# Performance work log

Hardware: AMD Instinct MI355X
Metric: run time of the kernel (lower is better)

## Reference

```python
import jax, jax.numpy as jnp
import numpy as np

N_NODES = 100000
N_EDGES = 20000
NNZ = 600000
N_GRAPHS = 64
IN_C, HID_C, OUT_C = 128, 128, 16


def setup_inputs() -> dict:
    key = jax.random.key(0)
    ks = jax.random.split(key, 10)
    x = jax.random.normal(ks[0], (N_NODES, IN_C), dtype=jnp.float32)
    node_idx = jax.random.randint(ks[1], (NNZ,), 0, N_NODES)
    edge_idx = jax.random.randint(ks[2], (NNZ,), 0, N_EDGES)
    batch = jnp.sort(jax.random.randint(ks[3], (N_NODES,), 0, N_GRAPHS))
    s1 = 1.0 / np.sqrt(IN_C)
    s2 = 1.0 / np.sqrt(HID_C)
    W1 = jax.random.uniform(ks[4], (IN_C, HID_C), jnp.float32, -s1, s1)
    b1 = jnp.zeros((HID_C,), jnp.float32)
    W2 = jax.random.uniform(ks[5], (HID_C, HID_C), jnp.float32, -s2, s2)
    b2 = jnp.zeros((HID_C,), jnp.float32)
    Wfc = jax.random.uniform(ks[6], (HID_C, OUT_C), jnp.float32, -s2, s2)
    bfc = jax.random.uniform(ks[7], (OUT_C,), jnp.float32, -s2, s2)
    return {"x": x, "node_idx": node_idx, "edge_idx": edge_idx, "batch": batch,
            "W1": W1, "b1": b1, "W2": W2, "b2": b2, "Wfc": Wfc, "bfc": bfc}


def hypergraph_conv(x, node_idx, edge_idx, W, b):
    # x' = D^{-1} H B^{-1} H^T (x W) + b   (unit hyperedge weights)
    x = x @ W  # lin has bias=False in PyG HypergraphConv
    ones = jnp.ones((node_idx.shape[0],), x.dtype)
    De = jax.ops.segment_sum(ones, edge_idx, num_segments=N_EDGES)   # hyperedge degree
    Dn = jax.ops.segment_sum(ones, node_idx, num_segments=N_NODES)  # node degree
    Binv = jnp.where(De > 0, 1.0 / De, 0.0)[:, None]
    Dinv = jnp.where(Dn > 0, 1.0 / Dn, 0.0)[:, None]
    # node -> hyperedge aggregation
    e = jax.ops.segment_sum(x[node_idx], edge_idx, num_segments=N_EDGES) * Binv
    # hyperedge -> node aggregation
    out = jax.ops.segment_sum(e[edge_idx], node_idx, num_segments=N_NODES) * Dinv
    return out + b


def reference(x, node_idx, edge_idx, batch, W1, b1, W2, b2, Wfc, bfc):
    h = jax.nn.relu(hypergraph_conv(x, node_idx, edge_idx, W1, b1))
    h = jax.nn.relu(hypergraph_conv(h, node_idx, edge_idx, W2, b2))
    # global mean pool over graphs
    cnt = jax.ops.segment_sum(jnp.ones((N_NODES,), h.dtype), batch, num_segments=N_GRAPHS)
    pooled = jax.ops.segment_sum(h, batch, num_segments=N_GRAPHS) / jnp.maximum(cnt, 1.0)[:, None]
    logits = pooled @ Wfc + bfc
    return jax.nn.log_softmax(logits, axis=1)
```

## Files before the change

### kernel.cpp

```cpp
#include <hip/hip_runtime.h>

#define N_NODES  100000
#define N_EDGES  20000
#define NNZ_     600000
#define N_GRAPHS 64
#define C_       128

typedef unsigned short ushort_t;
typedef unsigned int   uint_t;
typedef unsigned char  uchar_t;
typedef __attribute__((ext_vector_type(4))) float f32x4;
typedef __attribute__((ext_vector_type(2))) float f32x2;

__device__ __forceinline__ ushort_t f2bf(float f) {
    uint_t u = __float_as_uint(f);
    u += 0x7fffu + ((u >> 16) & 1u);
    return (ushort_t)(u >> 16);
}


#define SORT_ITEMS 2048
#define BKT_CAP    16384
#define NBKT_E     40
#define NBKT_N     49
#define SB_        ((NNZ_ + SORT_ITEMS - 1) / SORT_ITEMS)
#define CONV_XBLKS 6250
#define CONV_WBLKS 64

__global__ __launch_bounds__(256) void scatter_conv(const int* __restrict__ node_idx,
                                                    const int* __restrict__ edge_idx,
                                                    int* __restrict__ bcur,
                                                    int2* __restrict__ stage_e,
                                                    int2* __restrict__ stage_n,
                                                    const float* __restrict__ X, uint_t* __restrict__ X8,
                                                    const float* __restrict__ W1, const float* __restrict__ W2,
                                                    uchar_t* __restrict__ WT1, uchar_t* __restrict__ WT2) {
    __shared__ int cnt[NBKT_N];
    __shared__ int base[NBKT_N];
    __shared__ int gbase[NBKT_N];
    __shared__ int2 buf[SORT_ITEMS];
    int t = threadIdx.x;
    int bxx = blockIdx.x;

    if (bxx >= SB_) {
        int bx = bxx - SB_;
        if (bx < CONV_XBLKS) {
            size_t c = (size_t)bx * 256 + t;
            size_t bb = c * 8;
            if (bb >= (size_t)N_NODES * C_) return;
            float4 f0 = *(const float4*)(X + bb);
            float4 f1 = *(const float4*)(X + bb + 4);
            uint_t w0 = 0, w1 = 0;
            w0 = __builtin_amdgcn_cvt_pk_fp8_f32(f0.x, f0.y, w0, 0);
            w0 = __builtin_amdgcn_cvt_pk_fp8_f32(f0.z, f0.w, w0, 1);
            w1 = __builtin_amdgcn_cvt_pk_fp8_f32(f1.x, f1.y, w1, 0);
            w1 = __builtin_amdgcn_cvt_pk_fp8_f32(f1.z, f1.w, w1, 1);
            uint2 o; o.x = w0; o.y = w1;
            *(uint2*)(X8 + c * 2) = o;
        } else {
            bx -= CONV_XBLKS;
            const float* W = (bx < 32) ? W1 : W2;
            uchar_t* WT    = (bx < 32) ? WT1 : WT2;
            int idx = (bx & 31) * 256 + t;
            int n = idx >> 6, k2 = (idx & 63) * 2;
            float a = W[k2 * 128 + n];
            float b = W[(k2 + 1) * 128 + n];
            uint_t p = __builtin_amdgcn_cvt_pk_fp8_f32(a, b, 0, 0);
            *(ushort_t*)(WT + n * 128 + k2) = (ushort_t)(p & 0xffff);
        }
        return;
    }

    int start = bxx * SORT_ITEMS;
    int nitems = min(SORT_ITEMS, NNZ_ - start);

    int ek[8], nk[8];
    #pragma unroll
    for (int j = 0; j < 8; j++) {
        int i = t + j * 256;
        if (i < nitems) { ek[j] = edge_idx[start + i]; nk[j] = node_idx[start + i]; }
    }

    #pragma unroll
    for (int side = 0; side < 2; side++) {
        const int SHIFT = side ? 11 : 9;
        const int NBKT  = side ? NBKT_N : NBKT_E;
        int2* stage = side ? stage_n : stage_e;
        int*  bc    = bcur + side * 64;

        if (side) __syncthreads();
        for (int i = t; i < NBKT; i += 256) cnt[i] = 0;
        __syncthreads();

        int rank[8], bkt[8];
        #pragma unroll
        for (int j = 0; j < 8; j++) {
            int i = t + j * 256;
            if (i < nitems) {
                int key = side ? nk[j] : ek[j];
                bkt[j]  = key >> SHIFT;
                rank[j] = atomicAdd(&cnt[bkt[j]], 1);
            }
        }
        __syncthreads();
        if (t < 64) {
            int v = (t < NBKT) ? cnt[t] : 0;
            int s = v;
            #pragma unroll
            for (int o = 1; o < 64; o <<= 1) { int u = __shfl_up(s, o); if (t >= o) s += u; }
            if (t < NBKT) base[t] = s - v;
        }
        __syncthreads();
        if (t < NBKT) {
            int c = cnt[t];
            gbase[t] = t * BKT_CAP + ((c > 0) ? atomicAdd(&bc[t], c) : 0);
        }
        #pragma unroll
        for (int j = 0; j < 8; j++) {
            int i = t + j * 256;
            if (i < nitems) {
                int key = side ? nk[j] : ek[j];
                int val = side ? ek[j] : nk[j];
                buf[base[bkt[j]] + rank[j]] = make_int2(key, val);
            }
        }
        __syncthreads();
        for (int i = t; i < nitems; i += 256) {
            int2 p = buf[i];
            int b = p.x >> SHIFT;
            stage[gbase[b] + (i - base[b])] = p;
        }
    }
}

__global__ __launch_bounds__(1024) void bucket_build(const int2* __restrict__ stage_e,
                                                     const int2* __restrict__ stage_n,
                                                     const int* __restrict__ bcur,
                                                     int* __restrict__ ecnt, int* __restrict__ ncnt,
                                                     int* __restrict__ eoffs, int* __restrict__ noffs,
                                                     float* __restrict__ binv, float* __restrict__ dinv,
                                                     int* __restrict__ csr_en, int* __restrict__ csr_ne) {
    __shared__ int hist[2048];
    __shared__ int offs[2048];
    __shared__ int wsum[16];
    __shared__ int sbase;
    int t = threadIdx.x;
    int bx = blockIdx.x;
    const int2* sb; int* cnt; int* koffs; float* inv; int* csr;
    const int* bc; int b, width, nkeys, nb, k0;
    if (bx < NBKT_E) {
        b = bx; bc = bcur;
        sb = stage_e + (size_t)b * BKT_CAP; cnt = ecnt; koffs = eoffs; inv = binv; csr = csr_en;
        k0 = b << 9; width = 512; nkeys = N_EDGES; nb = NBKT_E;
    } else {
        b = bx - NBKT_E; bc = bcur + 64;
        sb = stage_n + (size_t)b * BKT_CAP; cnt = ncnt; koffs = noffs; inv = dinv; csr = csr_ne;
        k0 = b << 11; width = 2048; nkeys = N_NODES; nb = NBKT_N;
    }
    int n = bc[b];
    if (t < 64) {
        int v = (t < nb) ? bc[t] : 0;
        int s = v;
        #pragma unroll
        for (int o = 1; o < 64; o <<= 1) { int u = __shfl_up(s, o); if (t >= o) s += u; }
        if (t == b) sbase = s - v;
    }
    for (int i = t; i < width; i += 1024) hist[i] = 0;
    __syncthreads();
    for (int i = t; i < n; i += 1024) atomicAdd(&hist[sb[i].x - k0], 1);
    __syncthreads();
    int e0 = 0, e1 = 0;
    if (2 * t < width) { e0 = hist[2 * t]; e1 = hist[2 * t + 1]; }
    int s = e0 + e1;
    int lane = t & 63, wv = t >> 6;
    int sc = s;
    #pragma unroll
    for (int o = 1; o < 64; o <<= 1) { int u = __shfl_up(sc, o); if (lane >= o) sc += u; }
    if (lane == 63) wsum[wv] = sc;
    __syncthreads();
    if (t < 16) {
        int v = wsum[t];
        int s2 = v;
        #pragma unroll
        for (int o = 1; o < 16; o <<= 1) { int u = __shfl_up(s2, o); if (t >= o) s2 += u; }
        wsum[t] = s2 - v;
    }
    __syncthreads();
    if (2 * t < width) {
        int excl = (sc - s) + wsum[wv];
        offs[2 * t]     = excl;
        offs[2 * t + 1] = excl + e0;
    }
    __syncthreads();
    int base_g = sbase;
    for (int i = t; i < width; i += 1024) {
        int k = k0 + i;
        if (k < nkeys) {
            int c = hist[i];
            cnt[k]   = c;
            koffs[k] = base_g + offs[i];
            inv[k]   = (c > 0) ? 1.0f / (float)c : 0.0f;
        }
    }
    __syncthreads();
    for (int i = t; i < n; i += 1024) {
        int2 p = sb[i];
        int pos = atomicAdd(&offs[p.x - k0], 1);
        csr[base_g + pos] = p.y;
    }
}


__global__ __launch_bounds__(256) void gemm_mfma8(const uchar_t* __restrict__ A8,
                                                  const uchar_t* __restrict__ WT8,
                                                  uchar_t* __restrict__ C8, int M) {
    __shared__ __align__(16) uchar_t Wl[128 * 128];
    __shared__ __align__(16) uchar_t Al[64 * 128];
    int t = threadIdx.x;
    int r0 = blockIdx.x * 64;

    const uint4* WTg = (const uint4*)WT8;
    #pragma unroll
    for (int i = 0; i < 4; i++) {
        int c = i * 256 + t;
        int row = c >> 3, col16 = (c & 7) * 16;
        *(uint4*)&Wl[row * 128 + (col16 ^ ((row & 7) << 4))] = WTg[c];
    }
    #pragma unroll
    for (int i = 0; i < 2; i++) {
        int c = i * 256 + t;
        int row = c >> 3, col16 = (c & 7) * 16;
        int gr = r0 + row; if (gr >= M) gr = M - 1;
        uint4 v = *(const uint4*)(A8 + (size_t)gr * 128 + col16);
        *(uint4*)&Al[row * 128 + (col16 ^ ((row & 7) << 4))] = v;
    }
    __syncthreads();

    int lane = t & 63, wid = t >> 6;
    int arow = wid * 16 + (lane & 15);
    int kq = lane >> 4;
    f32x4 acc[8] = {};

    #pragma unroll
    for (int ks = 0; ks < 4; ks++) {
        int colb = ks * 32 + kq * 8;
        long a = *(const long*)&Al[arow * 128 + (colb ^ ((arow & 7) << 4))];
        #pragma unroll
        for (int nt = 0; nt < 8; nt++) {
            int wr = nt * 16 + (lane & 15);
            long b = *(const long*)&Wl[wr * 128 + (colb ^ ((wr & 7) << 4))];
            acc[nt] = __builtin_amdgcn_mfma_f32_16x16x32_fp8_fp8(a, b, acc[nt], 0, 0, 0);
        }
    }

    __syncthreads();
    uchar_t* Cl = Al;
    #pragma unroll
    for (int nt = 0; nt < 8; nt++) {
        int col = nt * 16 + (lane & 15);
        #pragma unroll
        for (int j = 0; j < 4; j++) {
            int rl = wid * 16 + kq * 4 + j;
            uint_t p = __builtin_amdgcn_cvt_pk_fp8_f32(acc[nt][j], acc[nt][j], 0, 0);
            Cl[rl * 128 + col] = (uchar_t)(p & 0xff);
        }
    }
    __syncthreads();
    int rows_here = min(64, M - r0);
    uint4* dst = (uint4*)(C8 + (size_t)r0 * 128);
    const uint4* src = (const uint4*)Cl;
    for (int c = t; c < rows_here * 8; c += 256) dst[c] = src[c];
}


__device__ __forceinline__ void acc16(uint4 v, float* a) {
    f32x2 p0 = __builtin_amdgcn_cvt_pk_f32_fp8(v.x, 0);
    f32x2 p1 = __builtin_amdgcn_cvt_pk_f32_fp8(v.x, 1);
    f32x2 p2 = __builtin_amdgcn_cvt_pk_f32_fp8(v.y, 0);
    f32x2 p3 = __builtin_amdgcn_cvt_pk_f32_fp8(v.y, 1);
    f32x2 p4 = __builtin_amdgcn_cvt_pk_f32_fp8(v.z, 0);
    f32x2 p5 = __builtin_amdgcn_cvt_pk_f32_fp8(v.z, 1);
    f32x2 p6 = __builtin_amdgcn_cvt_pk_f32_fp8(v.w, 0);
    f32x2 p7 = __builtin_amdgcn_cvt_pk_f32_fp8(v.w, 1);
    a[0] += p0.x;  a[1] += p0.y;  a[2] += p1.x;  a[3] += p1.y;
    a[4] += p2.x;  a[5] += p2.y;  a[6] += p3.x;  a[7] += p3.y;
    a[8] += p4.x;  a[9] += p4.y;  a[10] += p5.x; a[11] += p5.y;
    a[12] += p6.x; a[13] += p6.y; a[14] += p7.x; a[15] += p7.y;
}

__device__ __forceinline__ uint4 pack16(const float* r) {
    uint_t w0 = __builtin_amdgcn_cvt_pk_fp8_f32(r[0],  r[1],  0, 0);
    w0 = __builtin_amdgcn_cvt_pk_fp8_f32(r[2],  r[3],  w0, 1);
    uint_t w1 = __builtin_amdgcn_cvt_pk_fp8_f32(r[4],  r[5],  0, 0);
    w1 = __builtin_amdgcn_cvt_pk_fp8_f32(r[6],  r[7],  w1, 1);
    uint_t w2 = __builtin_amdgcn_cvt_pk_fp8_f32(r[8],  r[9],  0, 0);
    w2 = __builtin_amdgcn_cvt_pk_fp8_f32(r[10], r[11], w2, 1);
    uint_t w3 = __builtin_amdgcn_cvt_pk_fp8_f32(r[12], r[13], 0, 0);
    w3 = __builtin_amdgcn_cvt_pk_fp8_f32(r[14], r[15], w3, 1);
    uint4 o; o.x = w0; o.y = w1; o.z = w2; o.w = w3;
    return o;
}

__global__ __launch_bounds__(256) void gather_edges8(const uint4* __restrict__ X,
                                                     const int* __restrict__ csr,
                                                     const int* __restrict__ off, const int* __restrict__ cnt,
                                                     const float* __restrict__ binv,
                                                     uint4* __restrict__ E8) {
    int g = (blockIdx.x * blockDim.x + threadIdx.x) >> 3;
    int l = threadIdx.x & 7;
    if (g >= N_EDGES) return;
    int s = off[g], n = cnt[g];
    float a[16] = {};
    int i = 0;
    for (; i + 8 <= n; i += 8) {
        int r0 = csr[s + i],     r1 = csr[s + i + 1], r2 = csr[s + i + 2], r3 = csr[s + i + 3];
        int r4 = csr[s + i + 4], r5 = csr[s + i + 5], r6 = csr[s + i + 6], r7 = csr[s + i + 7];
        uint4 v0 = X[(size_t)r0 * 8 + l];
        uint4 v1 = X[(size_t)r1 * 8 + l];
        uint4 v2 = X[(size_t)r2 * 8 + l];
        uint4 v3 = X[(size_t)r3 * 8 + l];
        uint4 v4 = X[(size_t)r4 * 8 + l];
        uint4 v5 = X[(size_t)r5 * 8 + l];
        uint4 v6 = X[(size_t)r6 * 8 + l];
        uint4 v7 = X[(size_t)r7 * 8 + l];
        acc16(v0, a); acc16(v1, a); acc16(v2, a); acc16(v3, a);
        acc16(v4, a); acc16(v5, a); acc16(v6, a); acc16(v7, a);
    }
    for (; i + 4 <= n; i += 4) {
        int r0 = csr[s + i], r1 = csr[s + i + 1], r2 = csr[s + i + 2], r3 = csr[s + i + 3];
        uint4 v0 = X[(size_t)r0 * 8 + l];
        uint4 v1 = X[(size_t)r1 * 8 + l];
        uint4 v2 = X[(size_t)r2 * 8 + l];
        uint4 v3 = X[(size_t)r3 * 8 + l];
        acc16(v0, a); acc16(v1, a); acc16(v2, a); acc16(v3, a);
    }
    for (; i < n; i++) {
        uint4 v = X[(size_t)csr[s + i] * 8 + l];
        acc16(v, a);
    }
    float sc = binv[g];
    float r[16];
    #pragma unroll
    for (int j = 0; j < 16; j++) r[j] = a[j] * sc;
    E8[(size_t)g * 8 + l] = pack16(r);
}

__global__ __launch_bounds__(256) void gather_nodes8(const uint4* __restrict__ F,
                                                     const int* __restrict__ csr,
                                                     const int* __restrict__ off, const int* __restrict__ cnt,
                                                     const float* __restrict__ dinv,
                                                     const float* __restrict__ bias,
                                                     uint4* __restrict__ Y) {
    int g = (blockIdx.x * blockDim.x + threadIdx.x) >> 3;
    int l = threadIdx.x & 7;
    if (g >= N_NODES) return;
    int s = off[g], n = cnt[g];
    float a[16] = {};
    int i = 0;
    for (; i + 4 <= n; i += 4) {
        int r0 = csr[s + i], r1 = csr[s + i + 1], r2 = csr[s + i + 2], r3 = csr[s + i + 3];
        uint4 v0 = F[(size_t)r0 * 8 + l];
        uint4 v1 = F[(size_t)r1 * 8 + l];
        uint4 v2 = F[(size_t)r2 * 8 + l];
        uint4 v3 = F[(size_t)r3 * 8 + l];
        acc16(v0, a); acc16(v1, a); acc16(v2, a); acc16(v3, a);
    }
    for (; i < n; i++) {
        uint4 v = F[(size_t)csr[s + i] * 8 + l];
        acc16(v, a);
    }
    float sc = dinv[g];
    const float4* bb = (const float4*)bias + l * 4;
    float4 b0 = bb[0], b1 = bb[1], b2 = bb[2], b3 = bb[3];
    float r[16];
    r[0]  = fmaxf(a[0]  * sc + b0.x, 0.f);
    r[1]  = fmaxf(a[1]  * sc + b0.y, 0.f);
    r[2]  = fmaxf(a[2]  * sc + b0.z, 0.f);
    r[3]  = fmaxf(a[3]  * sc + b0.w, 0.f);
    r[4]  = fmaxf(a[4]  * sc + b1.x, 0.f);
    r[5]  = fmaxf(a[5]  * sc + b1.y, 0.f);
    r[6]  = fmaxf(a[6]  * sc + b1.z, 0.f);
    r[7]  = fmaxf(a[7]  * sc + b1.w, 0.f);
    r[8]  = fmaxf(a[8]  * sc + b2.x, 0.f);
    r[9]  = fmaxf(a[9]  * sc + b2.y, 0.f);
    r[10] = fmaxf(a[10] * sc + b2.z, 0.f);
    r[11] = fmaxf(a[11] * sc + b2.w, 0.f);
    r[12] = fmaxf(a[12] * sc + b3.x, 0.f);
    r[13] = fmaxf(a[13] * sc + b3.y, 0.f);
    r[14] = fmaxf(a[14] * sc + b3.z, 0.f);
    r[15] = fmaxf(a[15] * sc + b3.w, 0.f);
    Y[(size_t)g * 8 + l] = pack16(r);
}


#define POOL_BLOCKS 1024

__global__ __launch_bounds__(256) void pool_kernel8(const ushort_t* __restrict__ H,
                                                    const int* __restrict__ batch,
                                                    float* __restrict__ P) {
    int wgid = blockIdx.x * 4 + (threadIdx.x >> 6);
    int lane = threadIdx.x & 63;
    const int NW = POOL_BLOCKS * 4;
    const int per = (N_NODES + NW - 1) / NW;
    int r0 = wgid * per;
    int r1 = min(r0 + per, N_NODES);
    if (r0 >= r1) return;
    float ax = 0.f, ay = 0.f;
    int g = batch[r0];
    int hiw = lane & 1;
    for (int r = r0; r < r1; r++) {
        int gr = batch[r];
        if (gr != g) {
            atomicAdd(&P[g * C_ + lane * 2],     ax);
            atomicAdd(&P[g * C_ + lane * 2 + 1], ay);
            ax = 0.f; ay = 0.f; g = gr;
        }
        uint_t v = ((const uint_t*)H)[(size_t)r * 32 + (lane >> 1)];
        f32x2 p = hiw ? __builtin_amdgcn_cvt_pk_f32_fp8(v, 1)
                      : __builtin_amdgcn_cvt_pk_f32_fp8(v, 0);
        ax += p.x; ay += p.y;
    }
    atomicAdd(&P[g * C_ + lane * 2],     ax);
    atomicAdd(&P[g * C_ + lane * 2 + 1], ay);
}

__device__ __forceinline__ int lower_bound_dev(const int* __restrict__ a, int n, int key) {
    int lo = 0, hi = n;
    while (lo < hi) { int mid = (lo + hi) >> 1; if (a[mid] < key) lo = mid + 1; else hi = mid; }
    return lo;
}

__global__ __launch_bounds__(1024) void final_kernel(const float* __restrict__ P, const int* __restrict__ batch,
                                                     const float* __restrict__ Wfc, const float* __restrict__ bfc,
                                                     float* __restrict__ out) {
    int t = threadIdx.x;
    int r = t >> 4, c = t & 15;
    int lo = lower_bound_dev(batch, N_NODES, r);
    int hi = lower_bound_dev(batch, N_NODES, r + 1);
    float cnt = (float)((hi - lo) > 0 ? (hi - lo) : 1);
    float acc = 0.f;
    #pragma unroll 8
    for (int k = 0; k < C_; k++) acc += P[r * C_ + k] * Wfc[k * 16 + c];
    float logit = acc / cnt + bfc[c];
    __shared__ float l[N_GRAPHS][16];
    l[r][c] = logit;
    __syncthreads();
    float m = -1e30f;
    #pragma unroll
    for (int k = 0; k < 16; k++) m = fmaxf(m, l[r][k]);
    float sum = 0.f;
    #pragma unroll
    for (int k = 0; k < 16; k++) sum += expf(l[r][k] - m);
    out[t] = logit - m - logf(sum);
}


extern "C" void kernel_launch(void* const* d_in, const int* in_sizes, int n_in,
                              void* d_out, int out_size, void* d_ws, size_t ws_size,
                              hipStream_t stream) {
    const float* x        = (const float*)d_in[0];
    const int*   node_idx = (const int*)  d_in[1];
    const int*   edge_idx = (const int*)  d_in[2];
    const int*   batch    = (const int*)  d_in[3];
    const float* W1       = (const float*)d_in[4];
    const float* b1       = (const float*)d_in[5];
    const float* W2       = (const float*)d_in[6];
    const float* b2       = (const float*)d_in[7];
    const float* Wfc      = (const float*)d_in[8];
    const float* bfc      = (const float*)d_in[9];
    float* out = (float*)d_out;

    char* ws = (char*)d_ws;
    size_t off = 0;
    auto alloc = [&](size_t bytes) -> char* {
        off = (off + 255) & ~(size_t)255;
        char* p = ws + off;
        off += bytes;
        return p;
    };

    uint_t* x8     = (uint_t*)  alloc((size_t)N_NODES * C_);
    uint_t* h8     = (uint_t*)  alloc((size_t)N_NODES * C_);
    uchar_t* Eb8   = (uchar_t*) alloc((size_t)N_EDGES * C_);
    uchar_t* Fb8   = (uchar_t*) alloc((size_t)N_EDGES * C_);
    uchar_t* wt1   = (uchar_t*) alloc((size_t)C_ * C_);
    uchar_t* wt2   = (uchar_t*) alloc((size_t)C_ * C_);
    int2*  stage_e = (int2*) alloc((size_t)NBKT_E * BKT_CAP * 8);
    int2*  stage_n = (int2*) alloc((size_t)NBKT_N * BKT_CAP * 8);
    int*   bcur   = (int*)  alloc((size_t)128 * 4);
    float* pooled = (float*)alloc((size_t)N_GRAPHS * C_ * 4);
    char*  zend   = ws + off;
    int*   ecnt   = (int*)  alloc((size_t)N_EDGES * 4);
    int*   ncnt   = (int*)  alloc((size_t)N_NODES * 4);
    int*   eoffs  = (int*)  alloc((size_t)N_EDGES * 4);
    int*   noffs  = (int*)  alloc((size_t)N_NODES * 4);
    int*   csr_en = (int*)  alloc((size_t)NNZ_ * 4);
    int*   csr_ne = (int*)  alloc((size_t)NNZ_ * 4);
    float* binv   = (float*)alloc((size_t)N_EDGES * 4);
    float* dinv   = (float*)alloc((size_t)N_NODES * 4);

    (void)hipMemsetAsync((void*)bcur, 0, (size_t)(zend - (char*)bcur), stream);

    scatter_conv<<<SB_ + CONV_XBLKS + CONV_WBLKS, 256, 0, stream>>>(
        node_idx, edge_idx, bcur, stage_e, stage_n, x, x8, W1, W2, wt1, wt2);
    bucket_build<<<NBKT_E + NBKT_N, 1024, 0, stream>>>(
        stage_e, stage_n, bcur, ecnt, ncnt, eoffs, noffs, binv, dinv, csr_en, csr_ne);

    const int GEB = (N_EDGES + 63) / 64;
    gather_edges8<<<N_EDGES * 8 / 256, 256, 0, stream>>>((const uint4*)x8, csr_en, eoffs, ecnt, binv,
                                                         (uint4*)Eb8);
    gemm_mfma8<<<GEB, 256, 0, stream>>>(Eb8, wt1, Fb8, N_EDGES);
    gather_nodes8<<<N_NODES * 8 / 256, 256, 0, stream>>>((const uint4*)Fb8, csr_ne, noffs, ncnt, dinv, b1,
                                                         (uint4*)h8);
    gather_edges8<<<N_EDGES * 8 / 256, 256, 0, stream>>>((const uint4*)h8, csr_en, eoffs, ecnt, binv,
                                                         (uint4*)Eb8);
    gemm_mfma8<<<GEB, 256, 0, stream>>>(Eb8, wt2, Fb8, N_EDGES);
    gather_nodes8<<<N_NODES * 8 / 256, 256, 0, stream>>>((const uint4*)Fb8, csr_ne, noffs, ncnt, dinv, b2,
                                                         (uint4*)x8);
    pool_kernel8<<<POOL_BLOCKS, 256, 0, stream>>>((const ushort_t*)x8, batch, pooled);
    final_kernel<<<1, 1024, 0, stream>>>(pooled, batch, Wfc, bfc, out);
}
```

Measured before the change: 157.7 us.

## Fuse final node gather with mean-pool accumulation via shared-memory partial sums

Replaces the last gather_nodes8 plus pool_kernel8 pair with one kernel. Each block gathers 32 nodes, applies scale, bias and ReLU, and accumulates the results into two per-graph shared buffers before a few global atomics. This removes the write and re-read of the final node features and one launch. The cost is many LDS atomics per node, and correctness relies on each 32-node block spanning at most two graphs, which holds only because batch is sorted and graphs are large.

New measurement: 202.9 us. 28.7% more time.

```diff
diff --git a/kernel.cpp b/kernel.cpp
--- a/kernel.cpp
+++ b/kernel.cpp
@@ -392,37 +392,76 @@
     Y[(size_t)g * 8 + l] = pack16(r);
 }
 
-
-#define POOL_BLOCKS 1024
-
-__global__ __launch_bounds__(256) void pool_kernel8(const ushort_t* __restrict__ H,
-                                                    const int* __restrict__ batch,
-                                                    float* __restrict__ P) {
-    int wgid = blockIdx.x * 4 + (threadIdx.x >> 6);
-    int lane = threadIdx.x & 63;
-    const int NW = POOL_BLOCKS * 4;
-    const int per = (N_NODES + NW - 1) / NW;
-    int r0 = wgid * per;
-    int r1 = min(r0 + per, N_NODES);
-    if (r0 >= r1) return;
-    float ax = 0.f, ay = 0.f;
-    int g = batch[r0];
-    int hiw = lane & 1;
-    for (int r = r0; r < r1; r++) {
-        int gr = batch[r];
-        if (gr != g) {
-            atomicAdd(&P[g * C_ + lane * 2],     ax);
-            atomicAdd(&P[g * C_ + lane * 2 + 1], ay);
-            ax = 0.f; ay = 0.f; g = gr;
-        }
-        uint_t v = ((const uint_t*)H)[(size_t)r * 32 + (lane >> 1)];
-        f32x2 p = hiw ? __builtin_amdgcn_cvt_pk_f32_fp8(v, 1)
-                      : __builtin_amdgcn_cvt_pk_f32_fp8(v, 0);
-        ax += p.x; ay += p.y;
-    }
-    atomicAdd(&P[g * C_ + lane * 2],     ax);
-    atomicAdd(&P[g * C_ + lane * 2 + 1], ay);
-}
+__global__ __launch_bounds__(256) void gather_nodes_pool(const uint4* __restrict__ F,
+                                                         const int* __restrict__ csr,
+                                                         const int* __restrict__ off,
+                                                         const int* __restrict__ cnt,
+                                                         const float* __restrict__ dinv,
+                                                         const float* __restrict__ bias,
+                                                         const int* __restrict__ batch,
+                                                         float* __restrict__ P) {
+    __shared__ float pbuf[2][C_];
+    int t = threadIdx.x;
+    int g0 = blockIdx.x * 32;
+    int g = g0 + (t >> 3);
+    int l = t & 7;
+    pbuf[t >> 7][t & 127] = 0.f;
+    __syncthreads();
+
+    int gfirst = batch[g0];
+    int glast  = batch[min(g0 + 31, N_NODES - 1)];
+
+    if (g < N_NODES) {
+        int s = off[g], n = cnt[g];
+        float a[16] = {};
+        int i = 0;
+        for (; i + 4 <= n; i += 4) {
+            int r0 = csr[s + i], r1 = csr[s + i + 1], r2 = csr[s + i + 2], r3 = csr[s + i + 3];
+            uint4 v0 = F[(size_t)r0 * 8 + l];
+            uint4 v1 = F[(size_t)r1 * 8 + l];
+            uint4 v2 = F[(size_t)r2 * 8 + l];
+            uint4 v3 = F[(size_t)r3 * 8 + l];
+            acc16(v0, a); acc16(v1, a); acc16(v2, a); acc16(v3, a);
+        }
+        for (; i < n; i++) {
+            uint4 v = F[(size_t)csr[s + i] * 8 + l];
+            acc16(v, a);
+        }
+        float sc = dinv[g];
+        const float4* bb = (const float4*)bias + l * 4;
+        float4 b0 = bb[0], b1 = bb[1], b2 = bb[2], b3 = bb[3];
+        float r[16];
+        r[0]  = fmaxf(a[0]  * sc + b0.x, 0.f);
+        r[1]  = fmaxf(a[1]  * sc + b0.y, 0.f);
+        r[2]  = fmaxf(a[2]  * sc + b0.z, 0.f);
+        r[3]  = fmaxf(a[3]  * sc + b0.w, 0.f);
+        r[4]  = fmaxf(a[4]  * sc + b1.x, 0.f);
+        r[5]  = fmaxf(a[5]  * sc + b1.y, 0.f);
+        r[6]  = fmaxf(a[6]  * sc + b1.z, 0.f);
+        r[7]  = fmaxf(a[7]  * sc + b1.w, 0.f);
+        r[8]  = fmaxf(a[8]  * sc + b2.x, 0.f);
+        r[9]  = fmaxf(a[9]  * sc + b2.y, 0.f);
+        r[10] = fmaxf(a[10] * sc + b2.z, 0.f);
+        r[11] = fmaxf(a[11] * sc + b2.w, 0.f);
+        r[12] = fmaxf(a[12] * sc + b3.x, 0.f);
+        r[13] = fmaxf(a[13] * sc + b3.y, 0.f);
+        r[14] = fmaxf(a[14] * sc + b3.z, 0.f);
+        r[15] = fmaxf(a[15] * sc + b3.w, 0.f);
+        int slot = (batch[g] == gfirst) ? 0 : 1;
+        #pragma unroll
+        for (int j = 0; j < 16; j++) atomicAdd(&pbuf[slot][l * 16 + j], r[j]);
+    }
+    __syncthreads();
+    if (t < C_) {
+        float v = pbuf[0][t];
+        if (v != 0.f) atomicAdd(&P[gfirst * C_ + t], v);
+    } else if (glast != gfirst) {
+        int c = t - C_;
+        float v = pbuf[1][c];
+        if (v != 0.f) atomicAdd(&P[glast * C_ + c], v);
+    }
+}
+
 
 __device__ __forceinline__ int lower_bound_dev(const int* __restrict__ a, int n, int key) {
     int lo = 0, hi = n;
@@ -515,8 +554,7 @@
     gather_edges8<<<N_EDGES * 8 / 256, 256, 0, stream>>>((const uint4*)h8, csr_en, eoffs, ecnt, binv,
                                                          (uint4*)Eb8);
     gemm_mfma8<<<GEB, 256, 0, stream>>>(Eb8, wt2, Fb8, N_EDGES);
-    gather_nodes8<<<N_NODES * 8 / 256, 256, 0, stream>>>((const uint4*)Fb8, csr_ne, noffs, ncnt, dinv, b2,
-                                                         (uint4*)x8);
-    pool_kernel8<<<POOL_BLOCKS, 256, 0, stream>>>((const ushort_t*)x8, batch, pooled);
+    gather_nodes_pool<<<(N_NODES + 31) / 32, 256, 0, stream>>>((const uint4*)Fb8, csr_ne, noffs, ncnt,
+                                                               dinv, b2, batch, pooled);
     final_kernel<<<1, 1024, 0, stream>>>(pooled, batch, Wfc, bfc, out);
 }
```
